# Kernel tuning notes

Hardware: AMD Instinct MI355X
Metric: run time of the kernel (lower is better)

Reference implementation:

```python
import jax, jax.numpy as jnp
import numpy as np

KERNEL = 3
PAD = KERNEL // 2


def setup_inputs() -> dict:
    key = jax.random.key(0)
    k1, k2, k3, k4 = jax.random.split(key, 4)
    B, Cin, Cout, D = 2, 32, 64, 64
    x = jax.random.normal(k1, (B, Cin, D, D, D), dtype=jnp.float32)
    mask = jax.random.randint(k2, (B, D, D, D), 0, 2).astype(jnp.bool_)
    fan_in = Cin * KERNEL ** 3
    bound = 1.0 / np.sqrt(fan_in)
    weight = jax.random.uniform(k3, (Cout, Cin, KERNEL, KERNEL, KERNEL),
                                dtype=jnp.float32, minval=-bound, maxval=bound)
    bias = jax.random.uniform(k4, (Cout,), dtype=jnp.float32, minval=-bound, maxval=bound)
    return {"x": x, "mask": mask, "weight": weight, "bias": bias}


def reference(x, mask, weight, bias):
    # Dense conv3d with 'same' padding, then zero out unoccupied voxels
    # (the CUDA warp kernel only computes occupied voxels; others are 0).
    out = jax.lax.conv_general_dilated(
        x, weight,
        window_strides=(1, 1, 1),
        padding=[(PAD, PAD)] * 3,
        dimension_numbers=("NCDHW", "OIDHW", "NCDHW"),
    )
    out = out + bias[None, :, None, None, None]
    return out * mask[:, None, :, :, :].astype(out.dtype)
```

## Files before the change

kernel.cpp:

```cpp
#include <hip/hip_runtime.h>
#include <stdint.h>


#define DD 64
#define CIN 32
#define COUT 64

typedef __bf16 bf16x8 __attribute__((ext_vector_type(8)));
typedef float f32x16 __attribute__((ext_vector_type(16)));

#define XT_BYTES (2u * 64u * 64u * 64u * 32u * 2u)
#define WPK_U16  (27 * 2 * 2 * 64 * 8)
#define WS_NEEDED (XT_BYTES + (size_t)WPK_U16 * 2)

__device__ __forceinline__ uint16_t f2bf(float f) {
    uint32_t u = __builtin_bit_cast(uint32_t, f);
    u += 0x7fffu + ((u >> 16) & 1u);
    return (uint16_t)(u >> 16);
}

__global__ void pack_weights(const float* __restrict__ w, uint16_t* __restrict__ wpk) {
    int flat = blockIdx.x * 256 + threadIdx.x;
    if (flat >= WPK_U16) return;
    int j   = flat & 7;
    int l   = (flat >> 3) & 63;
    int ct  = (flat >> 9) & 1;
    int cb  = (flat >> 10) & 1;
    int k27 = flat >> 11;
    int co = ct * 32 + (l & 31);
    int ci = cb * 16 + ((l >> 5) * 8) + j;
    wpk[flat] = f2bf(w[(co * CIN + ci) * 27 + k27]);
}

__global__ __launch_bounds__(256)
void transpose_x(const float* __restrict__ x, uint16_t* __restrict__ xt) {
    __shared__ uint16_t tile[2048];
    const int y = blockIdx.x, z = blockIdx.y, b = blockIdx.z;
    const int t = threadIdx.x;
    const int ci = t >> 3;
    const int xs = (t & 7) * 8;
    const float* src = x + ((((size_t)b * CIN + ci) * DD + z) * DD + y) * DD + xs;
    float4 v0 = *(const float4*)src;
    float4 v1 = *(const float4*)(src + 4);
    float vals[8] = {v0.x, v0.y, v0.z, v0.w, v1.x, v1.y, v1.z, v1.w};
#pragma unroll
    for (int e = 0; e < 8; ++e) {
        int xv = xs + e;
        int pos = xv * 32 + (((ci >> 3) ^ ((xv >> 1) & 3)) << 3) + (ci & 7);
        tile[pos] = f2bf(vals[e]);
    }
    __syncthreads();
    uint16_t* dst = xt + (((size_t)b * DD + z) * DD + y) * 2048;
    ((uint4*)dst)[t] = ((const uint4*)tile)[t];
}

__global__ __launch_bounds__(256, 3)
void conv_mfma(const uint16_t* __restrict__ xt, const uint16_t* __restrict__ wpk,
               const int* __restrict__ mask, const float* __restrict__ bias,
               float* __restrict__ out) {
    __shared__ __align__(16) unsigned char lds[12 * 4224];
    const int yp = blockIdx.x, z = blockIdx.y, b = blockIdx.z;
    const int y0 = yp * 2;
    const int tid = threadIdx.x;
    const int lane = tid & 63;
    const int w = tid >> 6;
    const int wy = w >> 1;
    const int wc = w & 1;

    for (int i = tid; i < 96; i += 256) {
        int row = i >> 3, side = (i >> 2) & 1, k = i & 3;
        *(uint4*)&lds[row * 4224 + side * 4160 + k * 16] = make_uint4(0, 0, 0, 0);
    }
    for (int i = w; i < 48; i += 4) {
        int row = i >> 2, kc = i & 3;
        int zz = z - 1 + (row >> 2);
        int yy = y0 - 1 + (row & 3);
        unsigned ldsoff = row * 4224u + 64u + kc * 1024u + lane * 16u;
        if (zz >= 0 && zz < DD && yy >= 0 && yy < DD) {
            const uint16_t* src = xt + (((size_t)b * DD + zz) * DD + yy) * 2048 + kc * 512 + lane * 8;
            *(uint4*)&lds[ldsoff] = *(const uint4*)src;
        } else {
            *(uint4*)&lds[ldsoff] = make_uint4(0, 0, 0, 0);
        }
    }
    __syncthreads();

    const int u = lane & 31;
    const int h = lane >> 5;
    const int y = y0 + wy;

    f32x16 acc0, acc1;
#pragma unroll
    for (int i = 0; i < 16; ++i) { acc0[i] = 0.0f; acc1[i] = 0.0f; }

    for (int k27 = 0; k27 < 27; ++k27) {
        const int kz = k27 / 9;
        const int kyx = k27 % 9;
        const int ky = kyx / 3;
        const int kx = kyx % 3;
        const unsigned rowbase = (unsigned)(kz * 4 + wy + ky) * 4224u;
        const int xl0 = u + kx;
        const int xl1 = 32 + u + kx;
        const unsigned s0 = (((unsigned)(xl0 - 1)) >> 1) & 3u;
        const unsigned s1 = (((unsigned)(xl1 - 1)) >> 1) & 3u;
#pragma unroll
        for (int cb = 0; cb < 2; ++cb) {
            bf16x8 av = *(const bf16x8*)(wpk + (size_t)((k27 * 2 + cb) * 2 + wc) * 512 + lane * 8);
            const unsigned chunk = (unsigned)(cb * 2 + h);
            bf16x8 bv0 = *(const bf16x8*)&lds[rowbase + xl0 * 64u + ((chunk ^ s0) << 4)];
            bf16x8 bv1 = *(const bf16x8*)&lds[rowbase + xl1 * 64u + ((chunk ^ s1) << 4)];
            acc0 = __builtin_amdgcn_mfma_f32_32x32x16_bf16(av, bv0, acc0, 0, 0, 0);
            acc1 = __builtin_amdgcn_mfma_f32_32x32x16_bf16(av, bv1, acc1, 0, 0, 0);
        }
    }

    const size_t mbase = (((size_t)b * DD + z) * DD + y) * DD;
    const float m0 = mask[mbase + u] ? 1.0f : 0.0f;
    const float m1 = mask[mbase + 32 + u] ? 1.0f : 0.0f;
#pragma unroll
    for (int r = 0; r < 16; ++r) {
        int co = wc * 32 + (r & 3) + 8 * (r >> 2) + 4 * h;
        float bs = bias[co];
        size_t o = ((size_t)b * COUT + co) * (DD * DD * DD) + (size_t)z * (DD * DD) + (size_t)y * DD;
        out[o + u]      = (acc0[r] + bs) * m0;
        out[o + 32 + u] = (acc1[r] + bs) * m1;
    }
}

#define CI_BLK 16
__global__ __launch_bounds__(256, 2)
void sparse_conv3d_f32(const float* __restrict__ x,
                       const int* __restrict__ mask,
                       const float* __restrict__ weight,
                       const float* __restrict__ bias,
                       float* __restrict__ out) {
    __shared__ float lds[9 * CI_BLK * 66];
    const int y = blockIdx.x, z = blockIdx.y, b = blockIdx.z;
    const int lane = threadIdx.x & 63;
    const int wave = __builtin_amdgcn_readfirstlane(threadIdx.x >> 6);
    float acc[16];
#pragma unroll
    for (int j = 0; j < 16; ++j) acc[j] = 0.0f;
    const int co0 = wave * 16;
    const float* wbase = weight + (size_t)co0 * (CIN * 27);
    for (int cb = 0; cb < 2; ++cb) {
        if (cb) __syncthreads();
        for (int i = wave; i < 9 * CI_BLK; i += 4) {
            const int r = i >> 4, ci_l = i & 15;
            const int zz = z + (r / 3) - 1, yy = y + (r % 3) - 1;
            const int ci = cb * CI_BLK + ci_l;
            float v = 0.0f;
            if (zz >= 0 && zz < DD && yy >= 0 && yy < DD)
                v = x[((((size_t)b * CIN + ci) * DD + zz) * DD + yy) * DD + lane];
            float* row = &lds[(size_t)i * 66];
            row[1 + lane] = v;
            if (lane == 0) { row[0] = 0.0f; row[65] = 0.0f; }
        }
        __syncthreads();
        for (int ci_l = 0; ci_l < CI_BLK; ++ci_l) {
            const int ci = cb * CI_BLK + ci_l;
#pragma unroll
            for (int kz = 0; kz < 3; ++kz) {
#pragma unroll
                for (int ky = 0; ky < 3; ++ky) {
                    const int r = kz * 3 + ky;
                    const float* xrow = &lds[(size_t)(r * CI_BLK + ci_l) * 66 + lane];
                    const float xv0 = xrow[0], xv1 = xrow[1], xv2 = xrow[2];
                    const float* wp = wbase + ci * 27 + kz * 9 + ky * 3;
#pragma unroll
                    for (int j = 0; j < 16; ++j) {
                        acc[j] += wp[(size_t)j * (CIN * 27) + 0] * xv0
                                + wp[(size_t)j * (CIN * 27) + 1] * xv1
                                + wp[(size_t)j * (CIN * 27) + 2] * xv2;
                    }
                }
            }
        }
    }
    const float m = mask[(((size_t)b * DD + z) * DD + y) * DD + lane] ? 1.0f : 0.0f;
#pragma unroll
    for (int j = 0; j < 16; ++j) {
        const int co = co0 + j;
        out[((((size_t)b * COUT + co) * DD + z) * DD + y) * DD + lane] = (acc[j] + bias[co]) * m;
    }
}

extern "C" void kernel_launch(void* const* d_in, const int* in_sizes, int n_in,
                              void* d_out, int out_size, void* d_ws, size_t ws_size,
                              hipStream_t stream) {
    const float* x    = (const float*)d_in[0];
    const int*   mask = (const int*)d_in[1];
    const float* w    = (const float*)d_in[2];
    const float* bias = (const float*)d_in[3];
    float*       out  = (float*)d_out;

    if (ws_size < WS_NEEDED) {
        sparse_conv3d_f32<<<dim3(DD, DD, 2), 256, 0, stream>>>(x, mask, w, bias, out);
        return;
    }

    uint16_t* xt  = (uint16_t*)d_ws;
    uint16_t* wpk = (uint16_t*)((char*)d_ws + XT_BYTES);

    pack_weights<<<(WPK_U16 + 255) / 256, 256, 0, stream>>>(w, wpk);
    transpose_x<<<dim3(DD, DD, 2), 256, 0, stream>>>(x, xt);
    conv_mfma<<<dim3(DD / 2, DD, 2), 256, 0, stream>>>(xt, wpk, mask, bias, out);
}
```

Before: 107.0 us.

## Give each conv wave all 64 output channels and tile four y-rows per block

The conv block now covers four y rows instead of two. Each wave computes one y row for all 64 output channels using four accumulators, so every LDS-loaded input fragment feeds two MFMAs. The kz/ky/kx loops are unrolled. The halo-row overhead per output row drops from 2x to 1.5x, and LDS input reads per MFMA are halved. In exchange, register pressure and dynamic LDS (about 76KB) rise, occupancy drops to 2 blocks, and the grid has half as many blocks.

```diff
diff --git a/kernel.cpp b/kernel.cpp
--- a/kernel.cpp
+++ b/kernel.cpp
@@ -12,6 +12,7 @@
 #define XT_BYTES (2u * 64u * 64u * 64u * 32u * 2u)
 #define WPK_U16  (27 * 2 * 2 * 64 * 8)
 #define WS_NEEDED (XT_BYTES + (size_t)WPK_U16 * 2)
+#define CONV_LDS  (18 * 4224)
 
 __device__ __forceinline__ uint16_t f2bf(float f) {
     uint32_t u = __builtin_bit_cast(uint32_t, f);
@@ -54,63 +55,64 @@
     ((uint4*)dst)[t] = ((const uint4*)tile)[t];
 }
 
-__global__ __launch_bounds__(256, 3)
+__global__ __launch_bounds__(256, 2)
 void conv_mfma(const uint16_t* __restrict__ xt, const uint16_t* __restrict__ wpk,
                const int* __restrict__ mask, const float* __restrict__ bias,
                float* __restrict__ out) {
-    __shared__ __align__(16) unsigned char lds[12 * 4224];
-    const int yp = blockIdx.x, z = blockIdx.y, b = blockIdx.z;
-    const int y0 = yp * 2;
+    extern __shared__ __align__(16) unsigned char lds[];
+    const int yq = blockIdx.x, z = blockIdx.y, b = blockIdx.z;
+    const int y0 = yq * 4;
     const int tid = threadIdx.x;
     const int lane = tid & 63;
-    const int w = tid >> 6;
-    const int wy = w >> 1;
-    const int wc = w & 1;
-
-    for (int i = tid; i < 96; i += 256) {
+    const int w = __builtin_amdgcn_readfirstlane(tid >> 6);
+
+    for (int i = tid; i < 144; i += 256) {
         int row = i >> 3, side = (i >> 2) & 1, k = i & 3;
         *(uint4*)&lds[row * 4224 + side * 4160 + k * 16] = make_uint4(0, 0, 0, 0);
     }
-    for (int i = w; i < 48; i += 4) {
+    for (int i = w; i < 72; i += 4) {
         int row = i >> 2, kc = i & 3;
-        int zz = z - 1 + (row >> 2);
-        int yy = y0 - 1 + (row & 3);
-        unsigned ldsoff = row * 4224u + 64u + kc * 1024u + lane * 16u;
-        if (zz >= 0 && zz < DD && yy >= 0 && yy < DD) {
-            const uint16_t* src = xt + (((size_t)b * DD + zz) * DD + yy) * 2048 + kc * 512 + lane * 8;
-            *(uint4*)&lds[ldsoff] = *(const uint4*)src;
-        } else {
-            *(uint4*)&lds[ldsoff] = make_uint4(0, 0, 0, 0);
-        }
+        int zz = z - 1 + (row / 6);
+        int yy = y0 - 1 + (row % 6);
+        uint4 v = make_uint4(0, 0, 0, 0);
+        if (zz >= 0 && zz < DD && yy >= 0 && yy < DD)
+            v = *(const uint4*)(xt + (((size_t)b * DD + zz) * DD + yy) * 2048 + kc * 512 + lane * 8);
+        *(uint4*)&lds[row * 4224u + 64u + kc * 1024u + lane * 16u] = v;
     }
     __syncthreads();
 
     const int u = lane & 31;
     const int h = lane >> 5;
-    const int y = y0 + wy;
-
-    f32x16 acc0, acc1;
-#pragma unroll
-    for (int i = 0; i < 16; ++i) { acc0[i] = 0.0f; acc1[i] = 0.0f; }
-
-    for (int k27 = 0; k27 < 27; ++k27) {
-        const int kz = k27 / 9;
-        const int kyx = k27 % 9;
-        const int ky = kyx / 3;
-        const int kx = kyx % 3;
-        const unsigned rowbase = (unsigned)(kz * 4 + wy + ky) * 4224u;
-        const int xl0 = u + kx;
-        const int xl1 = 32 + u + kx;
-        const unsigned s0 = (((unsigned)(xl0 - 1)) >> 1) & 3u;
-        const unsigned s1 = (((unsigned)(xl1 - 1)) >> 1) & 3u;
-#pragma unroll
-        for (int cb = 0; cb < 2; ++cb) {
-            bf16x8 av = *(const bf16x8*)(wpk + (size_t)((k27 * 2 + cb) * 2 + wc) * 512 + lane * 8);
-            const unsigned chunk = (unsigned)(cb * 2 + h);
-            bf16x8 bv0 = *(const bf16x8*)&lds[rowbase + xl0 * 64u + ((chunk ^ s0) << 4)];
-            bf16x8 bv1 = *(const bf16x8*)&lds[rowbase + xl1 * 64u + ((chunk ^ s1) << 4)];
-            acc0 = __builtin_amdgcn_mfma_f32_32x32x16_bf16(av, bv0, acc0, 0, 0, 0);
-            acc1 = __builtin_amdgcn_mfma_f32_32x32x16_bf16(av, bv1, acc1, 0, 0, 0);
+    const int y = y0 + w;
+
+    f32x16 acc00, acc01, acc10, acc11;
+#pragma unroll
+    for (int i = 0; i < 16; ++i) { acc00[i] = 0.f; acc01[i] = 0.f; acc10[i] = 0.f; acc11[i] = 0.f; }
+
+    for (int kz = 0; kz < 3; ++kz) {
+#pragma unroll
+        for (int ky = 0; ky < 3; ++ky) {
+            const unsigned rowbase = (unsigned)((kz * 6 + w + ky) * 4224);
+#pragma unroll
+            for (int kx = 0; kx < 3; ++kx) {
+                const int k27 = (kz * 3 + ky) * 3 + kx;
+                const int xl0 = u + kx;
+                const int xl1 = 32 + u + kx;
+                const unsigned s0 = (((unsigned)(xl0 - 1)) >> 1) & 3u;
+                const unsigned s1 = (((unsigned)(xl1 - 1)) >> 1) & 3u;
+#pragma unroll
+                for (int cb = 0; cb < 2; ++cb) {
+                    const unsigned chunk = (unsigned)(cb * 2 + h);
+                    bf16x8 a0 = *(const bf16x8*)(wpk + (size_t)((k27 * 2 + cb) * 2 + 0) * 512 + lane * 8);
+                    bf16x8 a1 = *(const bf16x8*)(wpk + (size_t)((k27 * 2 + cb) * 2 + 1) * 512 + lane * 8);
+                    bf16x8 b0 = *(const bf16x8*)&lds[rowbase + xl0 * 64u + ((chunk ^ s0) << 4)];
+                    bf16x8 b1 = *(const bf16x8*)&lds[rowbase + xl1 * 64u + ((chunk ^ s1) << 4)];
+                    acc00 = __builtin_amdgcn_mfma_f32_32x32x16_bf16(a0, b0, acc00, 0, 0, 0);
+                    acc01 = __builtin_amdgcn_mfma_f32_32x32x16_bf16(a0, b1, acc01, 0, 0, 0);
+                    acc10 = __builtin_amdgcn_mfma_f32_32x32x16_bf16(a1, b0, acc10, 0, 0, 0);
+                    acc11 = __builtin_amdgcn_mfma_f32_32x32x16_bf16(a1, b1, acc11, 0, 0, 0);
+                }
+            }
         }
     }
 
@@ -118,12 +120,17 @@
     const float m0 = mask[mbase + u] ? 1.0f : 0.0f;
     const float m1 = mask[mbase + 32 + u] ? 1.0f : 0.0f;
 #pragma unroll
-    for (int r = 0; r < 16; ++r) {
-        int co = wc * 32 + (r & 3) + 8 * (r >> 2) + 4 * h;
-        float bs = bias[co];
-        size_t o = ((size_t)b * COUT + co) * (DD * DD * DD) + (size_t)z * (DD * DD) + (size_t)y * DD;
-        out[o + u]      = (acc0[r] + bs) * m0;
-        out[o + 32 + u] = (acc1[r] + bs) * m1;
+    for (int ct = 0; ct < 2; ++ct) {
+        const f32x16 A0 = ct ? acc10 : acc00;
+        const f32x16 A1 = ct ? acc11 : acc01;
+#pragma unroll
+        for (int r = 0; r < 16; ++r) {
+            int co = ct * 32 + (r & 3) + 8 * (r >> 2) + 4 * h;
+            float bs = bias[co];
+            size_t o = ((size_t)b * COUT + co) * (DD * DD * DD) + (size_t)z * (DD * DD) + (size_t)y * DD;
+            out[o + u]      = (A0[r] + bs) * m0;
+            out[o + 32 + u] = (A1[r] + bs) * m1;
+        }
     }
 }
 
@@ -204,5 +211,5 @@
 
     pack_weights<<<(WPK_U16 + 255) / 256, 256, 0, stream>>>(w, wpk);
     transpose_x<<<dim3(DD, DD, 2), 256, 0, stream>>>(x, xt);
-    conv_mfma<<<dim3(DD / 2, DD, 2), 256, 0, stream>>>(xt, wpk, mask, bias, out);
-}
+    conv_mfma<<<dim3(DD / 4, DD, 2), 256, CONV_LDS, stream>>>(xt, wpk, mask, bias, out);
+}
```

Result: slower. 152.5 us (+42.6%).
